# Performance work log

Measured on AMD Instinct MI355X. Metric: run time of the kernel, lower is better.

The kernel has to match this reference:

```python
import jax, jax.numpy as jnp
import numpy as np

BN_EPS = 1e-5

def conv1x1(x, w, b):
    # x: [B,C,H,W], w: [O,C], b: [O]
    return jnp.einsum('bchw,oc->bohw', x, w) + b[None, :, None, None]

def bn_inf(x, gamma, beta, mean, var):
    inv = gamma / jnp.sqrt(var + BN_EPS)
    return (x - mean[None, :, None, None]) * inv[None, :, None, None] + beta[None, :, None, None]

def setup_inputs() -> dict:
    key = jax.random.key(0)
    ks = jax.random.split(key, 24)
    B, Fg, Fl, Fi = 8, 256, 256, 64
    H = W = 64
    c8 = Fi // 8
    d = {}
    d['g'] = jax.random.normal(ks[0], (B, Fg, H, W), jnp.float32)
    d['x'] = jax.random.normal(ks[1], (B, Fl, H, W), jnp.float32)
    # W_g: conv1x1 + BN
    d['Wg_w'] = jax.random.normal(ks[2], (Fi, Fg), jnp.float32) * (1.0 / np.sqrt(Fg))
    d['Wg_b'] = jax.random.normal(ks[3], (Fi,), jnp.float32) * 0.02
    d['bng_gamma'] = jax.random.uniform(ks[4], (Fi,), jnp.float32, 0.5, 1.5)
    d['bng_beta'] = jax.random.normal(ks[5], (Fi,), jnp.float32) * 0.1
    d['bng_mean'] = jax.random.normal(ks[6], (Fi,), jnp.float32) * 0.1
    d['bng_var'] = jax.random.uniform(ks[7], (Fi,), jnp.float32, 0.5, 1.5)
    # W_x: conv1x1 + BN
    d['Wx_w'] = jax.random.normal(ks[8], (Fi, Fl), jnp.float32) * (1.0 / np.sqrt(Fl))
    d['Wx_b'] = jax.random.normal(ks[9], (Fi,), jnp.float32) * 0.02
    d['bnx_gamma'] = jax.random.uniform(ks[10], (Fi,), jnp.float32, 0.5, 1.5)
    d['bnx_beta'] = jax.random.normal(ks[11], (Fi,), jnp.float32) * 0.1
    d['bnx_mean'] = jax.random.normal(ks[12], (Fi,), jnp.float32) * 0.1
    d['bnx_var'] = jax.random.uniform(ks[13], (Fi,), jnp.float32, 0.5, 1.5)
    # psi: conv1x1 (Fi->1) + BN(1) + sigmoid
    d['psi_w'] = jax.random.normal(ks[14], (1, Fi), jnp.float32) * (1.0 / np.sqrt(Fi))
    d['psi_b'] = jax.random.normal(ks[15], (1,), jnp.float32) * 0.02
    d['bnp_gamma'] = jax.random.uniform(ks[16], (1,), jnp.float32, 0.5, 1.5)
    d['bnp_beta'] = jax.random.normal(ks[17], (1,), jnp.float32) * 0.1
    d['bnp_mean'] = jax.random.normal(ks[18], (1,), jnp.float32) * 0.1
    d['bnp_var'] = jax.random.uniform(ks[19], (1,), jnp.float32, 0.5, 1.5)
    # PAM convs
    d['pb_w'] = jax.random.normal(ks[20], (c8, Fi), jnp.float32) * (1.0 / np.sqrt(Fi))
    d['pb_b'] = jnp.zeros((c8,), jnp.float32)
    d['pc_w'] = jax.random.normal(ks[21], (c8, Fi), jnp.float32) * (1.0 / np.sqrt(Fi))
    d['pc_b'] = jnp.zeros((c8,), jnp.float32)
    d['pd_w'] = jax.random.normal(ks[22], (Fi, Fi), jnp.float32) * (1.0 / np.sqrt(Fi))
    d['pd_b'] = jnp.zeros((Fi,), jnp.float32)
    # scalar gates (torch inits to 0; use small nonzero to exercise the path)
    d['alpha'] = jax.random.normal(ks[23], (1,), jnp.float32) * 0.05
    d['cam_beta'] = jax.random.normal(jax.random.fold_in(key, 99), (1,), jnp.float32) * 0.05
    return d

def _cam(psi, cam_beta):
    B, C, H, W = psi.shape
    feat = psi.reshape(B, C, H * W)                       # [B,C,HW]
    att = jnp.einsum('bcn,bdn->bcd', feat, feat)          # [B,C,C]
    att_new = jnp.max(att, axis=-1, keepdims=True) - att  # max-subtract trick
    att = jax.nn.softmax(att_new, axis=-1)
    out = jnp.einsum('bcd,bdn->bcn', att, feat).reshape(B, C, H, W)
    return cam_beta[0] * out + psi

def _pam(psi, pb_w, pb_b, pc_w, pc_b, pd_w, pd_b, alpha):
    B, C, H, W = psi.shape
    HW = H * W
    fb = conv1x1(psi, pb_w, pb_b).reshape(B, -1, HW)      # [B,C/8,HW]
    fc = conv1x1(psi, pc_w, pc_b).reshape(B, -1, HW)      # [B,C/8,HW]
    energy = jnp.einsum('bki,bkj->bij', fb, fc)           # [B,HW,HW]
    att = jax.nn.softmax(energy, axis=-1)
    fd = conv1x1(psi, pd_w, pd_b).reshape(B, C, HW)       # [B,C,HW]
    out = jnp.einsum('bcj,bij->bci', fd, att).reshape(B, C, H, W)
    return alpha[0] * out + psi

def reference(g, x, Wg_w, Wg_b, bng_gamma, bng_beta, bng_mean, bng_var,
              Wx_w, Wx_b, bnx_gamma, bnx_beta, bnx_mean, bnx_var,
              psi_w, psi_b, bnp_gamma, bnp_beta, bnp_mean, bnp_var,
              pb_w, pb_b, pc_w, pc_b, pd_w, pd_b, alpha, cam_beta):
    g1 = bn_inf(conv1x1(g, Wg_w, Wg_b), bng_gamma, bng_beta, bng_mean, bng_var)
    x1 = bn_inf(conv1x1(x, Wx_w, Wx_b), bnx_gamma, bnx_beta, bnx_mean, bnx_var)
    psi = jax.nn.relu(g1 + x1)                            # [B,F_int,H,W]
    cam = _cam(psi, cam_beta)
    pam = _pam(psi, pb_w, pb_b, pc_w, pc_b, pd_w, pd_b, alpha)
    gate = bn_inf(conv1x1(cam * pam, psi_w, psi_b), bnp_gamma, bnp_beta, bnp_mean, bnp_var)
    da = jax.nn.sigmoid(gate)                             # [B,1,H,W]
    return x * da
```

## Files before the change

### kernel.cpp

```cpp
#include <hip/hip_runtime.h>
#include <hip/hip_bf16.h>
#include <math.h>

#define BB 8
#define CIN 256
#define FI 64
#define HW 4096
#define C8 8
#define EPS 1e-5f
#define LOG2E 1.4426950408889634f

typedef __attribute__((ext_vector_type(8))) short bf16x8;
typedef __attribute__((ext_vector_type(4))) float f32x4;
typedef unsigned short u16;

static __device__ __forceinline__ u16 f2b(float x) {
    unsigned u = __builtin_bit_cast(unsigned, x);
    return (u16)((u + 0x8000u) >> 16);
}
static __device__ __forceinline__ unsigned cvtpk(float a, float b) {
    unsigned r;
    asm("v_cvt_pk_bf16_f32 %0, %1, %2" : "=v"(r) : "v"(a), "v"(b));
    return r;
}
static __device__ __forceinline__ float b2f(u16 v) {
    return __builtin_bit_cast(float, ((unsigned)v) << 16);
}

__global__ __launch_bounds__(256) void k_prep(
    const float* __restrict__ Wg, const float* __restrict__ Wgb,
    const float* __restrict__ gg, const float* __restrict__ gbeta,
    const float* __restrict__ gm, const float* __restrict__ gv,
    const float* __restrict__ Wx, const float* __restrict__ Wxb,
    const float* __restrict__ xg, const float* __restrict__ xbeta,
    const float* __restrict__ xm, const float* __restrict__ xv,
    const float* __restrict__ pbw, const float* __restrict__ pbb,
    const float* __restrict__ pcw, const float* __restrict__ pcb,
    const float* __restrict__ pdw, const float* __restrict__ pdb,
    u16* __restrict__ Wp, float* __restrict__ Cp,
    u16* __restrict__ Wcat, float* __restrict__ bcat)
{
    const int gid = blockIdx.x * 256 + threadIdx.x;
    for (int idx = gid; idx < FI * 512; idx += 4096) {
        int o = idx >> 9, k = idx & 511;
        float s, w;
        if (k < 256) { s = gg[o] * rsqrtf(gv[o] + EPS); w = Wg[o * 256 + k]; }
        else         { s = xg[o] * rsqrtf(xv[o] + EPS); w = Wx[o * 256 + k - 256]; }
        Wp[idx] = f2b(w * s);
    }
    for (int idx = gid; idx < 80 * 64; idx += 4096) {
        int row = idx >> 6, col = idx & 63;
        float w;
        if (row < 8)       w = pbw[row * 64 + col] * LOG2E;
        else if (row < 16) w = pcw[(row - 8) * 64 + col];
        else               w = pdw[(row - 16) * 64 + col];
        Wcat[idx] = f2b(w);
    }
    if (blockIdx.x == 0) {
        int tid = threadIdx.x;
        if (tid < FI) {
            float ig = gg[tid] * rsqrtf(gv[tid] + EPS);
            float ix = xg[tid] * rsqrtf(xv[tid] + EPS);
            Cp[tid] = (Wgb[tid] - gm[tid]) * ig + gbeta[tid]
                    + (Wxb[tid] - xm[tid]) * ix + xbeta[tid];
        }
        if (tid >= 64 && tid < 144) {
            int r = tid - 64;
            float bv = (r < 8) ? pbb[r] * LOG2E : (r < 16 ? pcb[r - 8] : pdb[r - 16]);
            bcat[r] = bv;
        }
    }
}

__global__ __launch_bounds__(256) void k_psi(
    const float* __restrict__ g, const float* __restrict__ x,
    const u16* __restrict__ Wp, const float* __restrict__ Cp,
    const u16* __restrict__ Wcat, const float* __restrict__ bcat,
    u16* __restrict__ psiB, u16* __restrict__ psiLo,
    u16* __restrict__ fbcT, u16* __restrict__ fdB)
{
    const int tid  = threadIdx.x;
    const int lane = tid & 63;
    const int w    = tid >> 6;
    const int n    = lane & 15;
    const int quad = lane >> 4;
    const int b    = blockIdx.y;
    const int p0   = blockIdx.x * 64;

    __shared__ u16 InT[64][72];
    __shared__ u16 Tbc[64][16];

    f32x4 acc[4];
#pragma unroll
    for (int mt = 0; mt < 4; ++mt) acc[mt] = (f32x4){0.f, 0.f, 0.f, 0.f};

    for (int kc = 0; kc < 8; ++kc) {
        const float* src = (kc < 4) ? g : x;
        const int ch0 = (kc & 3) * 64;
        __syncthreads();
#pragma unroll
        for (int r = 0; r < 4; ++r) {
            int ch = (tid >> 4) + r * 16;
            int px = (tid & 15) * 4;
            float4 v = *(const float4*)&src[((size_t)b * CIN + ch0 + ch) * HW + p0 + px];
            InT[px][ch]     = f2b(v.x);
            InT[px + 1][ch] = f2b(v.y);
            InT[px + 2][ch] = f2b(v.z);
            InT[px + 3][ch] = f2b(v.w);
        }
        __syncthreads();
#pragma unroll
        for (int ks = 0; ks < 2; ++ks) {
            const int kglob = kc * 64 + ks * 32;
            bf16x8 bfrag = *(const bf16x8*)&InT[w * 16 + n][ks * 32 + quad * 8];
#pragma unroll
            for (int mt = 0; mt < 4; ++mt) {
                bf16x8 af = *(const bf16x8*)&Wp[(mt * 16 + n) * 512 + kglob + quad * 8];
                acc[mt] = __builtin_amdgcn_mfma_f32_16x16x32_bf16(
                              af, bfrag, acc[mt], 0, 0, 0);
            }
        }
    }

    float pv[4][4];
#pragma unroll
    for (int mt = 0; mt < 4; ++mt)
#pragma unroll
        for (int r = 0; r < 4; ++r) {
            int c = mt * 16 + quad * 4 + r;
            float v = acc[mt][r] + Cp[c];
            v = v > 0.f ? v : 0.f;
            pv[mt][r] = v;
            u16 hb = f2b(v);
            size_t idx = ((size_t)b * FI + c) * HW + p0 + w * 16 + n;
            psiB[idx]  = hb;
            psiLo[idx] = f2b(v - b2f(hb));
        }
    __syncthreads();
#pragma unroll
    for (int mt = 0; mt < 4; ++mt) {
        *(unsigned*)&InT[w * 16 + n][mt * 16 + quad * 4]     = cvtpk(pv[mt][0], pv[mt][1]);
        *(unsigned*)&InT[w * 16 + n][mt * 16 + quad * 4 + 2] = cvtpk(pv[mt][2], pv[mt][3]);
    }
    __syncthreads();

    f32x4 facc[5];
#pragma unroll
    for (int nt = 0; nt < 5; ++nt) facc[nt] = (f32x4){0.f, 0.f, 0.f, 0.f};
#pragma unroll
    for (int ks = 0; ks < 2; ++ks) {
        bf16x8 af = *(const bf16x8*)&InT[w * 16 + n][ks * 32 + quad * 8];
#pragma unroll
        for (int nt = 0; nt < 5; ++nt) {
            bf16x8 bf = *(const bf16x8*)&Wcat[(nt * 16 + n) * FI + ks * 32 + quad * 8];
            facc[nt] = __builtin_amdgcn_mfma_f32_16x16x32_bf16(af, bf, facc[nt], 0, 0, 0);
        }
    }
    __syncthreads();

    {
        float bias = bcat[n];
#pragma unroll
        for (int r = 0; r < 4; ++r)
            Tbc[w * 16 + quad * 4 + r][n] = f2b(facc[0][r] + bias);
    }
#pragma unroll
    for (int nt = 1; nt < 5; ++nt) {
        int ch = (nt - 1) * 16 + n;
        float bias = bcat[nt * 16 + n];
        *(unsigned*)&InT[ch][w * 16 + quad * 4]     = cvtpk(facc[nt][0] + bias, facc[nt][1] + bias);
        *(unsigned*)&InT[ch][w * 16 + quad * 4 + 2] = cvtpk(facc[nt][2] + bias, facc[nt][3] + bias);
    }
    __syncthreads();
    {
        int row = tid >> 2, part = tid & 3;
        uint2 v = *(const uint2*)&Tbc[row][part * 4];
        *(uint2*)&fbcT[((size_t)b * HW + p0 + row) * 16 + part * 4] = v;
    }
#pragma unroll
    for (int rep = 0; rep < 2; ++rep) {
        int t = rep * 256 + tid;
        int ch = t >> 3, seg = t & 7;
        bf16x8 v = *(const bf16x8*)&InT[ch][seg * 8];
        *(bf16x8*)&fdB[((size_t)b * FI + ch) * HW + p0 + seg * 8] = v;
    }
}

__global__ __launch_bounds__(256) void k_gram(
    const u16* __restrict__ psiB, const u16* __restrict__ psiLo,
    float* __restrict__ Gp)
{
    const int tid  = threadIdx.x;
    const int lane = tid & 63;
    const int w    = tid >> 6;
    const int n    = lane & 15;
    const int quad = lane >> 4;
    const int s    = blockIdx.x;
    const int b    = blockIdx.y;
    const int zz   = blockIdx.z;

    f32x4 acc[2];
#pragma unroll
    for (int nt = 0; nt < 2; ++nt) acc[nt] = (f32x4){0.f, 0.f, 0.f, 0.f};

    for (int ks = 0; ks < 4; ++ks) {
        const int k0 = s * 128 + ks * 32;
        const size_t ra = ((size_t)b * FI + w * 16 + n) * HW + k0 + quad * 8;
        bf16x8 ah = *(const bf16x8*)&psiB[ra];
        bf16x8 al = *(const bf16x8*)&psiLo[ra];
#pragma unroll
        for (int nt = 0; nt < 2; ++nt) {
            const size_t rb = ((size_t)b * FI + zz * 32 + nt * 16 + n) * HW + k0 + quad * 8;
            bf16x8 bh = *(const bf16x8*)&psiB[rb];
            bf16x8 bl = *(const bf16x8*)&psiLo[rb];
            acc[nt] = __builtin_amdgcn_mfma_f32_16x16x32_bf16(ah, bh, acc[nt], 0, 0, 0);
            acc[nt] = __builtin_amdgcn_mfma_f32_16x16x32_bf16(ah, bl, acc[nt], 0, 0, 0);
            acc[nt] = __builtin_amdgcn_mfma_f32_16x16x32_bf16(al, bh, acc[nt], 0, 0, 0);
        }
    }
#pragma unroll
    for (int nt = 0; nt < 2; ++nt)
#pragma unroll
        for (int r = 0; r < 4; ++r) {
            int i = w * 16 + quad * 4 + r;
            Gp[(((size_t)s * 8 + b) * 64 + i) * 64 + zz * 32 + nt * 16 + n] = acc[nt][r];
        }
}

__global__ __launch_bounds__(256) void k_camsm(
    const float* __restrict__ Gp, float* __restrict__ att)
{
    const int tid = threadIdx.x, tx = tid & 63, ty = tid >> 6;
    const int b = blockIdx.x, i = blockIdx.y;
    __shared__ float part[4][64];

    float gs = 0.f;
#pragma unroll
    for (int j = 0; j < 8; ++j) {
        int s = ty * 8 + j;
        gs += Gp[(((size_t)s * 8 + b) * 64 + i) * 64 + tx];
    }
    part[ty][tx] = gs;
    __syncthreads();
    if (tid < 64) {
        float gsum = part[0][tx] + part[1][tx] + part[2][tx] + part[3][tx];
        float M = gsum;
#pragma unroll
        for (int msk = 1; msk < 64; msk <<= 1) M = fmaxf(M, __shfl_xor(M, msk));
        float a = M - gsum;
        float m2 = a;
#pragma unroll
        for (int msk = 1; msk < 64; msk <<= 1) m2 = fmaxf(m2, __shfl_xor(m2, msk));
        float p = __expf(a - m2);
        float ssum = p;
#pragma unroll
        for (int msk = 1; msk < 64; msk <<= 1) ssum += __shfl_xor(ssum, msk);
        att[((size_t)b * 64 + i) * 64 + tx] = p / ssum;
    }
}

__global__ __launch_bounds__(256) void k_pam(
    const u16* __restrict__ fbcT, const u16* __restrict__ fdB,
    u16* __restrict__ Opart, float* __restrict__ ml)
{
    const int tid  = threadIdx.x;
    const int lane = tid & 63;
    const int w    = tid >> 6;
    const int n    = lane & 15;
    const int quad = lane >> 4;
    const int b    = blockIdx.x;
    const int i0   = blockIdx.y * 64;
    const int p    = blockIdx.z;
    const int jstart = p * 32, jend = jstart + 32;

    __shared__ u16 Ks[2][68][8];
    __shared__ u16 Vs[2][64][64];
    __shared__ u16 Ps[4][16][64];

    if (tid < 16) {
        ((unsigned*)&Ks[0][64][0])[tid] = 0u;
        ((unsigned*)&Ks[1][64][0])[tid] = 0u;
    }

    bf16x8 qfrag = {};
    if (quad == 0)
        qfrag = *(const bf16x8*)&fbcT[((size_t)b * HW + i0 + w * 16 + n) * 16];

    const int kkey = tid >> 1, khalf = tid & 1;
    const int vch  = tid >> 3, vseg  = tid & 7;
    const int vslot = (vseg ^ (vch & 7)) << 3;
    const int pswz  = n & 7;

    const u16* kp = fbcT + ((size_t)b * HW + jstart * 64) * 16 + 8;
    const u16* vp = fdB + (size_t)b * FI * HW + jstart * 64;

    uint2 kreg = make_uint2(0u, 0u);
    bf16x8 vreg0, vreg1;
    if (tid < 128) kreg = *(const uint2*)(kp + (size_t)kkey * 16 + khalf * 4);
    vreg0 = *(const bf16x8*)(vp + (size_t)vch * HW + vseg * 8);
    vreg1 = *(const bf16x8*)(vp + (size_t)(32 + vch) * HW + vseg * 8);

    f32x4 oacc[4];
#pragma unroll
    for (int mt = 0; mt < 4; ++mt) oacc[mt] = (f32x4){0.f, 0.f, 0.f, 0.f};
    float m = -1e30f, l = 0.f;

    int cur = 0;
    for (int jc = jstart; jc < jend; ++jc) {
        if (tid < 128) *(uint2*)&Ks[cur][kkey][khalf * 4] = kreg;
        *(bf16x8*)&Vs[cur][vch][vslot]      = vreg0;
        *(bf16x8*)&Vs[cur][32 + vch][vslot] = vreg1;
        if (jc + 1 < jend) {
            kp += 64 * 16;
            vp += 64;
            if (tid < 128) kreg = *(const uint2*)(kp + (size_t)kkey * 16 + khalf * 4);
            vreg0 = *(const bf16x8*)(vp + (size_t)vch * HW + vseg * 8);
            vreg1 = *(const bf16x8*)(vp + (size_t)(32 + vch) * HW + vseg * 8);
        }
        __syncthreads();

        f32x4 s[4];
        __builtin_amdgcn_s_setprio(1);
#pragma unroll
        for (int mt = 0; mt < 4; ++mt) {
            bf16x8 af = *(const bf16x8*)&Ks[cur][mt * 16 + n + quad][0];
            s[mt] = __builtin_amdgcn_mfma_f32_16x16x32_bf16(
                        af, qfrag, (f32x4){0.f, 0.f, 0.f, 0.f}, 0, 0, 0);
        }
        __builtin_amdgcn_s_setprio(0);

        float cmax = -1e30f;
#pragma unroll
        for (int mt = 0; mt < 4; ++mt)
            cmax = fmaxf(cmax, fmaxf(fmaxf(s[mt][0], s[mt][1]),
                                     fmaxf(s[mt][2], s[mt][3])));
        cmax = fmaxf(cmax, __shfl_xor(cmax, 16));
        cmax = fmaxf(cmax, __shfl_xor(cmax, 32));

        if (__any(cmax > m + 8.f)) {
            float mnew  = fmaxf(m, cmax);
            float scale = __builtin_amdgcn_exp2f(m - mnew);
            l *= scale;
#pragma unroll
            for (int mt = 0; mt < 4; ++mt) {
                oacc[mt][0] *= scale; oacc[mt][1] *= scale;
                oacc[mt][2] *= scale; oacc[mt][3] *= scale;
            }
            m = mnew;
        }

        float psum = 0.f;
        unsigned pw[4][2];
#pragma unroll
        for (int mt = 0; mt < 4; ++mt) {
            float e0 = __builtin_amdgcn_exp2f(s[mt][0] - m);
            float e1 = __builtin_amdgcn_exp2f(s[mt][1] - m);
            float e2 = __builtin_amdgcn_exp2f(s[mt][2] - m);
            float e3 = __builtin_amdgcn_exp2f(s[mt][3] - m);
            psum += (e0 + e1) + (e2 + e3);
            pw[mt][0] = cvtpk(e0, e1);
            pw[mt][1] = cvtpk(e2, e3);
        }
        l += psum;

#pragma unroll
        for (int mt = 0; mt < 4; ++mt) {
            int so = (((mt * 2 + (quad >> 1)) ^ pswz) << 3) + ((quad & 1) << 2);
            *(uint2*)&Ps[w][n][so] = make_uint2(pw[mt][0], pw[mt][1]);
        }
        asm volatile("s_waitcnt lgkmcnt(0)" ::: "memory");
        __builtin_amdgcn_sched_barrier(0);

        __builtin_amdgcn_s_setprio(1);
#pragma unroll
        for (int k0 = 0; k0 < 2; ++k0) {
            bf16x8 pf = *(const bf16x8*)&Ps[w][n][((k0 * 4 + quad) ^ pswz) << 3];
#pragma unroll
            for (int mt = 0; mt < 4; ++mt) {
                bf16x8 vf = *(const bf16x8*)
                    &Vs[cur][mt * 16 + n][((k0 * 4 + quad) ^ pswz) << 3];
                oacc[mt] = __builtin_amdgcn_mfma_f32_16x16x32_bf16(
                               vf, pf, oacc[mt], 0, 0, 0);
            }
        }
        __builtin_amdgcn_s_setprio(0);
        cur ^= 1;
    }

    l += __shfl_xor(l, 16);
    l += __shfl_xor(l, 32);
    const float rl = 1.f / l;
#pragma unroll
    for (int mt = 0; mt < 4; ++mt)
#pragma unroll
        for (int r = 0; r < 4; ++r) {
            int c = mt * 16 + quad * 4 + r;
            Opart[(((size_t)p * 8 + b) * FI + c) * HW + i0 + w * 16 + n] =
                f2b(oacc[mt][r] * rl);
        }
    if (quad == 0)
        ((float2*)ml)[((size_t)p * 8 + b) * HW + i0 + w * 16 + n] = make_float2(m, l);
}

__global__ __launch_bounds__(256) void k_final(
    const u16* __restrict__ psiB, const u16* __restrict__ psiLo,
    const float* __restrict__ att,
    const u16* __restrict__ Opart, const float* __restrict__ ml,
    const float* __restrict__ x,
    const float* __restrict__ psiw, const float* __restrict__ psib,
    const float* __restrict__ pg, const float* __restrict__ pbeta,
    const float* __restrict__ pm, const float* __restrict__ pv,
    const float* __restrict__ alpha, const float* __restrict__ camb,
    float* __restrict__ out)
{
    const int tid  = threadIdx.x;
    const int lane = tid & 63;
    const int w    = tid >> 6;
    const int n    = lane & 15;
    const int quad = lane >> 4;
    const int b = blockIdx.y, p0 = blockIdx.x * 64;

    __shared__ u16 Abf[64][64];
    __shared__ u16 tpB[64][64];
    __shared__ u16 tpLo[64][64];
    __shared__ float Wc0[64], Wc1[64], Pw[64], daL[64];
    __shared__ float Zp[4][64];

    {
        int c = tid >> 2, seg = tid & 3;
        const float* ap = &att[((size_t)b * 64 + c) * 64 + seg * 16];
        float4 v0 = *(const float4*)(ap);
        float4 v1 = *(const float4*)(ap + 4);
        float4 v2 = *(const float4*)(ap + 8);
        float4 v3 = *(const float4*)(ap + 12);
        float vv[16] = {v0.x, v0.y, v0.z, v0.w, v1.x, v1.y, v1.z, v1.w,
                        v2.x, v2.y, v2.z, v2.w, v3.x, v3.y, v3.z, v3.w};
#pragma unroll
        for (int j = 0; j < 8; ++j) {
            int d0 = seg * 16 + j * 2;
            int phys = (((d0 >> 3) ^ (c & 7)) << 3) | (d0 & 7);
            *(unsigned*)&Abf[c][phys] = cvtpk(vv[2 * j], vv[2 * j + 1]);
        }
    }
    {
        int px = tid & 63, grp = tid >> 6;
#pragma unroll
        for (int cc = 0; cc < 16; cc += 2) {
            int c = grp * 16 + cc;
            size_t i0 = ((size_t)b * FI + c) * HW + p0 + px;
            unsigned hb = ((unsigned)psiB[i0]) | (((unsigned)psiB[i0 + HW]) << 16);
            unsigned lb = ((unsigned)psiLo[i0]) | (((unsigned)psiLo[i0 + HW]) << 16);
            int phys = (((c >> 3) ^ (px & 7)) << 3) | (c & 7);
            *(unsigned*)&tpB[px][phys]  = hb;
            *(unsigned*)&tpLo[px][phys] = lb;
        }
    }
    if (tid < 64) {
        Pw[tid] = psiw[tid];
        float2 ml0 = ((const float2*)ml)[((size_t)0 * 8 + b) * HW + p0 + tid];
        float2 ml1 = ((const float2*)ml)[((size_t)1 * 8 + b) * HW + p0 + tid];
        float M  = fmaxf(ml0.x, ml1.x);
        float w0 = ml0.y * __builtin_amdgcn_exp2f(ml0.x - M);
        float w1 = ml1.y * __builtin_amdgcn_exp2f(ml1.x - M);
        float winv = 1.f / (w0 + w1);
        Wc0[tid] = w0 * winv; Wc1[tid] = w1 * winv;
    }
    __syncthreads();

    f32x4 acc[4];
#pragma unroll
    for (int nt = 0; nt < 4; ++nt) acc[nt] = (f32x4){0.f, 0.f, 0.f, 0.f};
#pragma unroll
    for (int ks = 0; ks < 2; ++ks) {
        int arow = w * 16 + n;
        bf16x8 af = *(const bf16x8*)&Abf[arow][((ks * 4 + quad) ^ (arow & 7)) << 3];
#pragma unroll
        for (int nt = 0; nt < 4; ++nt) {
            int brow = nt * 16 + n;
            int boff = ((ks * 4 + quad) ^ (brow & 7)) << 3;
            bf16x8 bh = *(const bf16x8*)&tpB[brow][boff];
            bf16x8 bl = *(const bf16x8*)&tpLo[brow][boff];
            acc[nt] = __builtin_amdgcn_mfma_f32_16x16x32_bf16(af, bh, acc[nt], 0, 0, 0);
            acc[nt] = __builtin_amdgcn_mfma_f32_16x16x32_bf16(af, bl, acc[nt], 0, 0, 0);
        }
    }

    const float al = alpha[0], cb = camb[0];
    float z[4] = {0.f, 0.f, 0.f, 0.f};
#pragma unroll
    for (int nt = 0; nt < 4; ++nt) {
        int px = nt * 16 + n;
        float w0 = Wc0[px], w1 = Wc1[px];
#pragma unroll
        for (int r = 0; r < 4; ++r) {
            int c = w * 16 + quad * 4 + r;
            int phys = (((c >> 3) ^ (px & 7)) << 3) | (c & 7);
            float ps  = b2f(tpB[px][phys]) + b2f(tpLo[px][phys]);
            float cam = cb * acc[nt][r] + ps;
            float oa = w0 * b2f(Opart[(((size_t)0 * 8 + b) * FI + c) * HW + p0 + px])
                     + w1 * b2f(Opart[(((size_t)1 * 8 + b) * FI + c) * HW + p0 + px]);
            float pam = al * oa + ps;
            z[nt] += Pw[c] * (cam * pam);
        }
    }
#pragma unroll
    for (int nt = 0; nt < 4; ++nt) {
        z[nt] += __shfl_xor(z[nt], 16);
        z[nt] += __shfl_xor(z[nt], 32);
    }
    if (quad == 0) {
#pragma unroll
        for (int nt = 0; nt < 4; ++nt) Zp[w][nt * 16 + n] = z[nt];
    }
    __syncthreads();
    if (tid < 64) {
        float zt = Zp[0][tid] + Zp[1][tid] + Zp[2][tid] + Zp[3][tid] + psib[0];
        float inv = pg[0] * rsqrtf(pv[0] + EPS);
        float gate = (zt - pm[0]) * inv + pbeta[0];
        daL[tid] = 1.f / (1.f + __expf(-gate));
    }
    __syncthreads();

    const int tx = lane;
    const float da = daL[tx];
#pragma unroll 8
    for (int r = 0; r < 64; ++r) {
        int cl = w + 4 * r;
        size_t idx = ((size_t)b * CIN + cl) * HW + p0 + tx;
        out[idx] = x[idx] * da;
    }
}

extern "C" void kernel_launch(void* const* d_in, const int* in_sizes, int n_in,
                              void* d_out, int out_size, void* d_ws, size_t ws_size,
                              hipStream_t stream)
{
    const float* g     = (const float*)d_in[0];
    const float* x     = (const float*)d_in[1];
    const float* Wg_w  = (const float*)d_in[2];
    const float* Wg_b  = (const float*)d_in[3];
    const float* bng_g = (const float*)d_in[4];
    const float* bng_b = (const float*)d_in[5];
    const float* bng_m = (const float*)d_in[6];
    const float* bng_v = (const float*)d_in[7];
    const float* Wx_w  = (const float*)d_in[8];
    const float* Wx_b  = (const float*)d_in[9];
    const float* bnx_g = (const float*)d_in[10];
    const float* bnx_b = (const float*)d_in[11];
    const float* bnx_m = (const float*)d_in[12];
    const float* bnx_v = (const float*)d_in[13];
    const float* psi_w = (const float*)d_in[14];
    const float* psi_b = (const float*)d_in[15];
    const float* bnp_g = (const float*)d_in[16];
    const float* bnp_b = (const float*)d_in[17];
    const float* bnp_m = (const float*)d_in[18];
    const float* bnp_v = (const float*)d_in[19];
    const float* pb_w  = (const float*)d_in[20];
    const float* pb_b  = (const float*)d_in[21];
    const float* pc_w  = (const float*)d_in[22];
    const float* pc_b  = (const float*)d_in[23];
    const float* pd_w  = (const float*)d_in[24];
    const float* pd_b  = (const float*)d_in[25];
    const float* alpha = (const float*)d_in[26];
    const float* camb  = (const float*)d_in[27];
    float* out = (float*)d_out;

    float* ws   = (float*)d_ws;
    u16*  psiB  = (u16*)(ws);
    u16*  psiLo = (u16*)(ws + 1048576);
    u16*  fbcT  = (u16*)(ws + 2097152);
    u16*  fdB   = (u16*)(ws + 2359296);
    float* att  = ws + 3407872;
    u16*  Wp    = (u16*)(ws + 3440640);
    float* Cp   = ws + 3457024;
    u16*  Wcat  = (u16*)(ws + 3457088);
    float* bcat = ws + 3459648;
    float* mlws = ws + 3459744;
    float* Gp   = ws + 3590816;
    u16*  Opart = (u16*)(ws + 3590816);

    k_prep<<<dim3(16), 256, 0, stream>>>(Wg_w, Wg_b, bng_g, bng_b, bng_m, bng_v,
                                         Wx_w, Wx_b, bnx_g, bnx_b, bnx_m, bnx_v,
                                         pb_w, pb_b, pc_w, pc_b, pd_w, pd_b,
                                         Wp, Cp, Wcat, bcat);
    k_psi<<<dim3(64, 8), 256, 0, stream>>>(g, x, Wp, Cp, Wcat, bcat,
                                           psiB, psiLo, fbcT, fdB);
    k_gram<<<dim3(32, 8, 2), 256, 0, stream>>>(psiB, psiLo, Gp);
    k_camsm<<<dim3(8, 64), 256, 0, stream>>>(Gp, att);
    k_pam<<<dim3(8, 64, 2), 256, 0, stream>>>(fbcT, fdB, Opart, mlws);
    k_final<<<dim3(64, 8), 256, 0, stream>>>(psiB, psiLo, att, Opart, mlws, x,
                                             psi_w, psi_b, bnp_g, bnp_b, bnp_m, bnp_v,
                                             alpha, camb, out);
}
```

Baseline: 247.8 us.

## Unroll PAM attention loop by two with two-tile-deep register prefetch

Unrolls the flash-attention loop over key/value tiles by two, with fixed LDS buffers per half-step, and keeps two tiles of K/V in registers so global loads are issued two tiles ahead. It also removes the explicit lgkmcnt wait and sched_barrier between the P store and the PV MFMA, and reshapes the max reduction into a linear chain. The goal is to hide global-load latency and cut loop/indexing overhead. In exchange it uses more registers, assumes an even tile count per split, and drops the explicit LDS wait that ordered the P writes before the reads.

```diff
diff --git a/kernel.cpp b/kernel.cpp
--- a/kernel.cpp
+++ b/kernel.cpp
@@ -294,98 +294,116 @@
     const u16* kp = fbcT + ((size_t)b * HW + jstart * 64) * 16 + 8;
     const u16* vp = fdB + (size_t)b * FI * HW + jstart * 64;
 
-    uint2 kreg = make_uint2(0u, 0u);
-    bf16x8 vreg0, vreg1;
-    if (tid < 128) kreg = *(const uint2*)(kp + (size_t)kkey * 16 + khalf * 4);
-    vreg0 = *(const bf16x8*)(vp + (size_t)vch * HW + vseg * 8);
-    vreg1 = *(const bf16x8*)(vp + (size_t)(32 + vch) * HW + vseg * 8);
+    uint2 kr0 = make_uint2(0u, 0u), kr1 = make_uint2(0u, 0u);
+    bf16x8 v0a, v0b, v1a, v1b;
+    if (tid < 128) {
+        kr0 = *(const uint2*)(kp + (size_t)kkey * 16 + khalf * 4);
+        kr1 = *(const uint2*)(kp + 1024 + (size_t)kkey * 16 + khalf * 4);
+    }
+    v0a = *(const bf16x8*)(vp + (size_t)vch * HW + vseg * 8);
+    v0b = *(const bf16x8*)(vp + (size_t)(32 + vch) * HW + vseg * 8);
+    v1a = *(const bf16x8*)(vp + 64 + (size_t)vch * HW + vseg * 8);
+    v1b = *(const bf16x8*)(vp + 64 + (size_t)(32 + vch) * HW + vseg * 8);
 
     f32x4 oacc[4];
 #pragma unroll
     for (int mt = 0; mt < 4; ++mt) oacc[mt] = (f32x4){0.f, 0.f, 0.f, 0.f};
     float m = -1e30f, l = 0.f;
 
-    int cur = 0;
-    for (int jc = jstart; jc < jend; ++jc) {
-        if (tid < 128) *(uint2*)&Ks[cur][kkey][khalf * 4] = kreg;
-        *(bf16x8*)&Vs[cur][vch][vslot]      = vreg0;
-        *(bf16x8*)&Vs[cur][32 + vch][vslot] = vreg1;
-        if (jc + 1 < jend) {
-            kp += 64 * 16;
-            vp += 64;
-            if (tid < 128) kreg = *(const uint2*)(kp + (size_t)kkey * 16 + khalf * 4);
-            vreg0 = *(const bf16x8*)(vp + (size_t)vch * HW + vseg * 8);
-            vreg1 = *(const bf16x8*)(vp + (size_t)(32 + vch) * HW + vseg * 8);
+#define PAM_STEP(BUF)                                                           \
+    {                                                                           \
+        f32x4 s[4];                                                             \
+        __builtin_amdgcn_s_setprio(1);                                          \
+        _Pragma("unroll")                                                       \
+        for (int mt = 0; mt < 4; ++mt) {                                        \
+            bf16x8 af = *(const bf16x8*)&Ks[BUF][mt * 16 + n + quad][0];        \
+            s[mt] = __builtin_amdgcn_mfma_f32_16x16x32_bf16(                    \
+                        af, qfrag, (f32x4){0.f, 0.f, 0.f, 0.f}, 0, 0, 0);       \
+        }                                                                       \
+        __builtin_amdgcn_s_setprio(0);                                          \
+                               \
+        float cm = fmaxf(fmaxf(s[0][0], s[0][1]), s[0][2]);                     \
+        cm = fmaxf(fmaxf(cm, s[0][3]), s[1][0]);                                \
+        cm = fmaxf(fmaxf(cm, s[1][1]), s[1][2]);                                \
+        cm = fmaxf(fmaxf(cm, s[1][3]), s[2][0]);                                \
+        cm = fmaxf(fmaxf(cm, s[2][1]), s[2][2]);                                \
+        cm = fmaxf(fmaxf(cm, s[2][3]), s[3][0]);                                \
+        cm = fmaxf(fmaxf(cm, s[3][1]), s[3][2]);                                \
+        cm = fmaxf(cm, s[3][3]);                                                \
+        cm = fmaxf(cm, __shfl_xor(cm, 16));                                     \
+        cm = fmaxf(cm, __shfl_xor(cm, 32));                                     \
+        if (__any(cm > m + 8.f)) {                                              \
+            float mnew  = fmaxf(m, cm);                                         \
+            float scale = __builtin_amdgcn_exp2f(m - mnew);                     \
+            l *= scale;                                                         \
+            _Pragma("unroll")                                                   \
+            for (int mt = 0; mt < 4; ++mt) {                                    \
+                oacc[mt][0] *= scale; oacc[mt][1] *= scale;                     \
+                oacc[mt][2] *= scale; oacc[mt][3] *= scale;                     \
+            }                                                                   \
+            m = mnew;                                                           \
+        }                                                                       \
+        float psum = 0.f;                                                       \
+        unsigned pw[4][2];                                                      \
+        _Pragma("unroll")                                                       \
+        for (int mt = 0; mt < 4; ++mt) {                                        \
+            float e0 = __builtin_amdgcn_exp2f(s[mt][0] - m);                    \
+            float e1 = __builtin_amdgcn_exp2f(s[mt][1] - m);                    \
+            float e2 = __builtin_amdgcn_exp2f(s[mt][2] - m);                    \
+            float e3 = __builtin_amdgcn_exp2f(s[mt][3] - m);                    \
+            psum += (e0 + e1) + (e2 + e3);                                      \
+            pw[mt][0] = cvtpk(e0, e1);                                          \
+            pw[mt][1] = cvtpk(e2, e3);                                          \
+        }                                                                       \
+        l += psum;                                                              \
+        _Pragma("unroll")                                                       \
+        for (int mt = 0; mt < 4; ++mt) {                                        \
+            int so = (((mt * 2 + (quad >> 1)) ^ pswz) << 3) + ((quad & 1) << 2);\
+            *(uint2*)&Ps[w][n][so] = make_uint2(pw[mt][0], pw[mt][1]);          \
+        }                                                                       \
+        __builtin_amdgcn_s_setprio(1);                                          \
+        _Pragma("unroll")                                                       \
+        for (int k0 = 0; k0 < 2; ++k0) {                                        \
+            bf16x8 pf = *(const bf16x8*)&Ps[w][n][((k0 * 4 + quad) ^ pswz) << 3];\
+            _Pragma("unroll")                                                   \
+            for (int mt = 0; mt < 4; ++mt) {                                    \
+                bf16x8 vf = *(const bf16x8*)                                    \
+                    &Vs[BUF][mt * 16 + n][((k0 * 4 + quad) ^ pswz) << 3];       \
+                oacc[mt] = __builtin_amdgcn_mfma_f32_16x16x32_bf16(             \
+                               vf, pf, oacc[mt], 0, 0, 0);                      \
+            }                                                                   \
+        }                                                                       \
+        __builtin_amdgcn_s_setprio(0);                                          \
+    }
+
+    for (int jc = jstart; jc < jend; jc += 2) {
+        if (tid < 128) *(uint2*)&Ks[0][kkey][khalf * 4] = kr0;
+        *(bf16x8*)&Vs[0][vch][vslot]      = v0a;
+        *(bf16x8*)&Vs[0][32 + vch][vslot] = v0b;
+        if (jc + 2 < jend) {
+            if (tid < 128)
+                kr0 = *(const uint2*)(kp + 2048 + (size_t)kkey * 16 + khalf * 4);
+            v0a = *(const bf16x8*)(vp + 128 + (size_t)vch * HW + vseg * 8);
+            v0b = *(const bf16x8*)(vp + 128 + (size_t)(32 + vch) * HW + vseg * 8);
         }
         __syncthreads();
-
-        f32x4 s[4];
-        __builtin_amdgcn_s_setprio(1);
-#pragma unroll
-        for (int mt = 0; mt < 4; ++mt) {
-            bf16x8 af = *(const bf16x8*)&Ks[cur][mt * 16 + n + quad][0];
-            s[mt] = __builtin_amdgcn_mfma_f32_16x16x32_bf16(
-                        af, qfrag, (f32x4){0.f, 0.f, 0.f, 0.f}, 0, 0, 0);
-        }
-        __builtin_amdgcn_s_setprio(0);
-
-        float cmax = -1e30f;
-#pragma unroll
-        for (int mt = 0; mt < 4; ++mt)
-            cmax = fmaxf(cmax, fmaxf(fmaxf(s[mt][0], s[mt][1]),
-                                     fmaxf(s[mt][2], s[mt][3])));
-        cmax = fmaxf(cmax, __shfl_xor(cmax, 16));
-        cmax = fmaxf(cmax, __shfl_xor(cmax, 32));
-
-        if (__any(cmax > m + 8.f)) {
-            float mnew  = fmaxf(m, cmax);
-            float scale = __builtin_amdgcn_exp2f(m - mnew);
-            l *= scale;
-#pragma unroll
-            for (int mt = 0; mt < 4; ++mt) {
-                oacc[mt][0] *= scale; oacc[mt][1] *= scale;
-                oacc[mt][2] *= scale; oacc[mt][3] *= scale;
-            }
-            m = mnew;
-        }
-
-        float psum = 0.f;
-        unsigned pw[4][2];
-#pragma unroll
-        for (int mt = 0; mt < 4; ++mt) {
-            float e0 = __builtin_amdgcn_exp2f(s[mt][0] - m);
-            float e1 = __builtin_amdgcn_exp2f(s[mt][1] - m);
-            float e2 = __builtin_amdgcn_exp2f(s[mt][2] - m);
-            float e3 = __builtin_amdgcn_exp2f(s[mt][3] - m);
-            psum += (e0 + e1) + (e2 + e3);
-            pw[mt][0] = cvtpk(e0, e1);
-            pw[mt][1] = cvtpk(e2, e3);
-        }
-        l += psum;
-
-#pragma unroll
-        for (int mt = 0; mt < 4; ++mt) {
-            int so = (((mt * 2 + (quad >> 1)) ^ pswz) << 3) + ((quad & 1) << 2);
-            *(uint2*)&Ps[w][n][so] = make_uint2(pw[mt][0], pw[mt][1]);
-        }
-        asm volatile("s_waitcnt lgkmcnt(0)" ::: "memory");
-        __builtin_amdgcn_sched_barrier(0);
-
-        __builtin_amdgcn_s_setprio(1);
-#pragma unroll
-        for (int k0 = 0; k0 < 2; ++k0) {
-            bf16x8 pf = *(const bf16x8*)&Ps[w][n][((k0 * 4 + quad) ^ pswz) << 3];
-#pragma unroll
-            for (int mt = 0; mt < 4; ++mt) {
-                bf16x8 vf = *(const bf16x8*)
-                    &Vs[cur][mt * 16 + n][((k0 * 4 + quad) ^ pswz) << 3];
-                oacc[mt] = __builtin_amdgcn_mfma_f32_16x16x32_bf16(
-                               vf, pf, oacc[mt], 0, 0, 0);
-            }
-        }
-        __builtin_amdgcn_s_setprio(0);
-        cur ^= 1;
-    }
+        PAM_STEP(0)
+
+        if (tid < 128) *(uint2*)&Ks[1][kkey][khalf * 4] = kr1;
+        *(bf16x8*)&Vs[1][vch][vslot]      = v1a;
+        *(bf16x8*)&Vs[1][32 + vch][vslot] = v1b;
+        if (jc + 3 < jend) {
+            if (tid < 128)
+                kr1 = *(const uint2*)(kp + 3072 + (size_t)kkey * 16 + khalf * 4);
+            v1a = *(const bf16x8*)(vp + 192 + (size_t)vch * HW + vseg * 8);
+            v1b = *(const bf16x8*)(vp + 192 + (size_t)(32 + vch) * HW + vseg * 8);
+        }
+        kp += 2048;
+        vp += 128;
+        __syncthreads();
+        PAM_STEP(1)
+    }
+#undef PAM_STEP
 
     l += __shfl_xor(l, 16);
     l += __shfl_xor(l, 32);
```

New measurement: 244.9 us. About the same (-1.2%).
